# Kernel optimization log

Hardware: AMD Instinct MI355X
Metric: run time of the kernel (lower is better)

## Reference

```python
import jax, jax.numpy as jnp
import numpy as np
import math

DIM_MODEL = 1024
N_HEAD = 16
NUM_NEURON = 64
MAX_LEN = 2048
B, S = 4, 2048


def setup_inputs() -> dict:
    key = jax.random.key(0)
    ks = jax.random.split(key, 11)
    d, p = DIM_MODEL, N_HEAD * NUM_NEURON
    sc_in = 1.0 / math.sqrt(d)
    sc_p = 1.0 / math.sqrt(p)
    return {
        "q": jax.random.normal(ks[0], (B, S, d), jnp.float32),
        "k": jax.random.normal(ks[1], (B, S, d), jnp.float32),
        "v": jax.random.normal(ks[2], (B, S, d), jnp.float32),
        "Wq": jax.random.normal(ks[3], (d, p), jnp.float32) * sc_in,
        "bq": jnp.zeros((p,), jnp.float32),
        "Wk": jax.random.normal(ks[4], (d, p), jnp.float32) * sc_in,
        "bk": jnp.zeros((p,), jnp.float32),
        "Wv": jax.random.normal(ks[5], (d, p), jnp.float32) * sc_in,
        "bv": jnp.zeros((p,), jnp.float32),
        "Wf": jax.random.normal(ks[6], (p, d), jnp.float32) * sc_p,
        "bf": jnp.zeros((d,), jnp.float32),
    }


def _split_heads(x):  # [B,S,H*Dh] -> [B,H,S,Dh]
    b, s, _ = x.shape
    return x.reshape(b, s, N_HEAD, NUM_NEURON).transpose(0, 2, 1, 3)


def reference(q, k, v, Wq, bq, Wk, bk, Wv, bv, Wf, bf):
    qh = _split_heads(q @ Wq + bq)
    kh = _split_heads(k @ Wk + bk)
    vh = _split_heads(v @ Wv + bv)
    # NOTE: original scales by 1/sqrt(max_len), not 1/sqrt(head_dim)
    scores = jnp.einsum("bhqd,bhkd->bhqk", qh, kh) / math.sqrt(MAX_LEN)
    s = scores.shape[-1]
    causal = jnp.tril(jnp.ones((s, s), bool))  # [S,S]
    scores = jnp.where(causal[None, None], scores, -jnp.inf)
    attn = jax.nn.softmax(scores, axis=-1)
    out = jnp.einsum("bhqk,bhkd->bhqd", attn, vh)  # [B,H,S,Dh]
    c = out.transpose(0, 2, 1, 3).reshape(out.shape[0], out.shape[2], N_HEAD * NUM_NEURON)
    return c @ Wf + bf
```

## Files before the change

kernel.cpp:

```cpp
#include <hip/hip_runtime.h>
#include <stdint.h>

#define DMODEL 1024
#define NHEAD 16
#define DH 64
#define BB 4
#define SS 2048
#define MROWS (BB * SS)

typedef __bf16 bfx8 __attribute__((ext_vector_type(8)));
typedef float f32x4 __attribute__((ext_vector_type(4)));
typedef float fvec4 __attribute__((ext_vector_type(4)));
typedef int i32x4 __attribute__((ext_vector_type(4)));
typedef unsigned short u16x8 __attribute__((ext_vector_type(8)));
typedef unsigned short u16x4 __attribute__((ext_vector_type(4)));

__device__ __forceinline__ unsigned short f2bf(float f) {
    union { float f; unsigned int u; } v; v.f = f;
    unsigned int r = v.u + 0x7FFFu + ((v.u >> 16) & 1u);
    return (unsigned short)(r >> 16);
}

__device__ __forceinline__ unsigned int cvtpk(float lo, float hi) {
    unsigned int r;
    asm("v_cvt_pk_bf16_f32 %0, %1, %2" : "=v"(r) : "v"(lo), "v"(hi));
    return r;
}

typedef __attribute__((address_space(1))) const void gas_t;
typedef __attribute__((address_space(3))) void las_t;
__device__ __forceinline__ void gload_lds16(const void* g, void* l) {
    __builtin_amdgcn_global_load_lds((gas_t*)g, (las_t*)l, 16, 0, 0);
}

__device__ __forceinline__ int sigma_k(int i) {
    return (i & 0x20) | ((i & 0x0C) << 1) | ((i & 0x10) >> 2) | (i & 3);
}

__global__ void cvt3_kernel(const float* __restrict__ s0, const float* __restrict__ s1,
                            const float* __restrict__ s2,
                            unsigned short* __restrict__ d0, unsigned short* __restrict__ d1,
                            unsigned short* __restrict__ d2, int n8)
{
    const float* s = (blockIdx.y == 0) ? s0 : (blockIdx.y == 1) ? s1 : s2;
    unsigned short* d = (blockIdx.y == 0) ? d0 : (blockIdx.y == 1) ? d1 : d2;
    int i = blockIdx.x * blockDim.x + threadIdx.x;
    if (i >= n8) return;
    fvec4 a = *reinterpret_cast<const fvec4*>(&s[(size_t)i * 8]);
    fvec4 b = *reinterpret_cast<const fvec4*>(&s[(size_t)i * 8 + 4]);
    u16x8 o;
    #pragma unroll
    for (int j = 0; j < 4; ++j) { o[j] = f2bf(a[j]); o[j + 4] = f2bf(b[j]); }
    *reinterpret_cast<u16x8*>(&d[(size_t)i * 8]) = o;
}

__global__ void transpose_cvt3_kernel(const float* __restrict__ W0, unsigned short* __restrict__ T0,
                                      const float* __restrict__ W1, unsigned short* __restrict__ T1,
                                      const float* __restrict__ W2, unsigned short* __restrict__ T2)
{
    const float* W = (blockIdx.z == 0) ? W0 : (blockIdx.z == 1) ? W1 : W2;
    unsigned short* Wt = (blockIdx.z == 0) ? T0 : (blockIdx.z == 1) ? T1 : T2;
    __shared__ unsigned short t[64][72];
    const int tid = threadIdx.x;
    const int r0 = blockIdx.y * 64, c0 = blockIdx.x * 64;
    #pragma unroll
    for (int i = 0; i < 4; ++i) {
        int idx = tid + i * 256;
        int r = idx >> 4, c4 = idx & 15;
        fvec4 v = *reinterpret_cast<const fvec4*>(&W[(size_t)(r0 + r) * DMODEL + c0 + c4 * 4]);
        #pragma unroll
        for (int j = 0; j < 4; ++j) t[c4 * 4 + j][r] = f2bf(v[j]);
    }
    __syncthreads();
    #pragma unroll
    for (int i = 0; i < 2; ++i) {
        int idx = tid + i * 256;
        int r = idx >> 3, c8 = idx & 7;
        u16x8 v = *reinterpret_cast<const u16x8*>(&t[r][c8 * 8]);
        *reinterpret_cast<u16x8*>(&Wt[(size_t)(c0 + r) * DMODEL + r0 + c8 * 8]) = v;
    }
}

struct GArg {
    const unsigned short* A;
    const unsigned short* Bt;
    const float* bias;
    void* O;
    float osc;
    int mode;
};

__global__ __launch_bounds__(256, 4)
void gemm_kernel(GArg g0, GArg g1, int M, int N, int K)
{
    const GArg g = blockIdx.z ? g1 : g0;
    __shared__ unsigned short sA[128 * 64];
    __shared__ unsigned short sB[128 * 64];
    const int tid  = threadIdx.x;
    const int lane = tid & 63;
    const int wave = tid >> 6;
    const int wm = (wave >> 1) * 64, wn = (wave & 1) * 64;
    const int m0 = blockIdx.x * 128, n0 = blockIdx.y * 128;
    const int lr = lane & 15;
    const int lg = lane >> 4;

    f32x4 acc[4][4] = {};

    for (int kk0 = 0; kk0 < K; kk0 += 64) {
        __syncthreads();
        #pragma unroll
        for (int i = 0; i < 4; ++i) {
            int c = tid + i * 256;
            int row = c >> 3, col8 = c & 7;
            gload_lds16(&g.A[(size_t)(m0 + row) * K + kk0 + col8 * 8], &sA[c * 8]);
        }
        #pragma unroll
        for (int i = 0; i < 4; ++i) {
            int c = tid + i * 256;
            int row = c >> 3, col8 = c & 7;
            gload_lds16(&g.Bt[(size_t)(n0 + row) * K + kk0 + col8 * 8], &sB[c * 8]);
        }
        __syncthreads();

        #pragma unroll
        for (int kk = 0; kk < 2; ++kk) {
            bfx8 af[4], bfr[4];
            #pragma unroll
            for (int m = 0; m < 4; ++m)
                af[m] = *reinterpret_cast<const bfx8*>(
                    &sA[(wm + m * 16 + lr) * 64 + kk * 32 + lg * 8]);
            #pragma unroll
            for (int n = 0; n < 4; ++n)
                bfr[n] = *reinterpret_cast<const bfx8*>(
                    &sB[(wn + n * 16 + lr) * 64 + kk * 32 + lg * 8]);
            #pragma unroll
            for (int m = 0; m < 4; ++m)
                #pragma unroll
                for (int n = 0; n < 4; ++n)
                    acc[m][n] = __builtin_amdgcn_mfma_f32_16x16x32_bf16(
                        af[m], bfr[n], acc[m][n], 0, 0, 0);
        }
    }

    #pragma unroll
    for (int n = 0; n < 4; ++n) {
        int col = n0 + wn + n * 16 + lr;
        float bv = g.bias[col];
        #pragma unroll
        for (int m = 0; m < 4; ++m) {
            int rowb = m0 + wm + m * 16 + lg * 4;
            float val[4];
            #pragma unroll
            for (int r = 0; r < 4; ++r) val[r] = (acc[m][n][r] + bv) * g.osc;
            if (g.mode == 0) {
                #pragma unroll
                for (int r = 0; r < 4; ++r)
                    ((unsigned short*)g.O)[(size_t)(rowb + r) * N + col] = f2bf(val[r]);
            } else if (g.mode == 2) {
                #pragma unroll
                for (int r = 0; r < 4; ++r)
                    ((float*)g.O)[(size_t)(rowb + r) * N + col] = val[r];
            } else {
                int bq = rowb >> 11, s = rowb & 2047;
                int hh = col >> 6, d = col & 63;
                u16x4 pk;
                #pragma unroll
                for (int r = 0; r < 4; ++r) pk[r] = f2bf(val[r]);
                size_t idx = ((size_t)(bq * 16 + hh) * 64 + d) * 2048 + s;
                *reinterpret_cast<u16x4*>(&((unsigned short*)g.O)[idx]) = pk;
            }
        }
    }
}

__global__ __launch_bounds__(512, 4)
void attn_kernel(const unsigned short* __restrict__ Q,
                 const unsigned short* __restrict__ K,
                 const unsigned short* __restrict__ Vt,
                 unsigned short* __restrict__ C)
{
    __shared__ unsigned short sK[2][8192];
    __shared__ unsigned short sV[2][8192];

    const int tid  = threadIdx.x;
    const int lane = tid & 63;
    const int wave = tid >> 6;
    const int lr = lane & 15, lg = lane >> 4;
    const int bh = blockIdx.x;
    const int p  = blockIdx.y;
    const int b = bh >> 4, h = bh & 15;
    const size_t rowbase = (size_t)b * SS;
    const int hcol = h * DH;

    const int srow = tid >> 3, sc8 = tid & 7;
    const int sig  = sigma_k(srow);
    const int woff = srow * 64 + ((sc8 ^ (srow & 7)) * 8);
    const int p0 = lg ^ (lr & 7);

    const u16x8 onesu = {0x3F80, 0x3F80, 0x3F80, 0x3F80, 0x3F80, 0x3F80, 0x3F80, 0x3F80};
    union { u16x8 u; bfx8 b; } onesc; onesc.u = onesu;
    const bfx8 ones = onesc.b;

    #pragma unroll
    for (int ph = 0; ph < 2; ++ph) {
        const int qt = ph ? p : (15 - p);
        const int q0 = qt * 128;

        bfx8 aq[2];
        {
            int qr = q0 + wave * 16 + lr;
            const unsigned short* qp = &Q[(rowbase + qr) * DMODEL + hcol + lg * 8];
            aq[0] = *reinterpret_cast<const bfx8*>(qp);
            aq[1] = *reinterpret_cast<const bfx8*>(qp + 32);
        }

        float m_run = 0.f;
        f32x4 acc_l = {};
        f32x4 acc_o[4] = {};
        bool mz = true;
        const int qmax_wave = q0 + wave * 16 + 15;
        const int npairs = qt + 1;

        u16x8 rk[2], rv[2];
        #pragma unroll
        for (int s = 0; s < 2; ++s) {
            rk[s] = *reinterpret_cast<const u16x8*>(
                &K[(rowbase + s * 64 + sig) * DMODEL + hcol + sc8 * 8]);
            rv[s] = *reinterpret_cast<const u16x8*>(
                &Vt[((size_t)bh * DH + srow) * SS + s * 64 + sc8 * 8]);
        }
        #pragma unroll
        for (int s = 0; s < 2; ++s) {
            *reinterpret_cast<u16x8*>(&sK[0][s * 4096 + woff]) = rk[s];
            *reinterpret_cast<u16x8*>(&sV[0][s * 4096 + woff]) = rv[s];
        }
        if (npairs > 1) {
            #pragma unroll
            for (int s = 0; s < 2; ++s) {
                const int kk = (2 + s) * 64;
                rk[s] = *reinterpret_cast<const u16x8*>(
                    &K[(rowbase + kk + sig) * DMODEL + hcol + sc8 * 8]);
                rv[s] = *reinterpret_cast<const u16x8*>(
                    &Vt[((size_t)bh * DH + srow) * SS + kk + sc8 * 8]);
            }
        }
        __syncthreads();

        for (int u = 0; u < npairs; ++u) {
            const int cur = u & 1;
            #pragma unroll
            for (int s = 0; s < 2; ++s) {
                const int k0 = (2 * u + s) * 64;
                if (k0 > qmax_wave) break;

                f32x4 sc[4];
                __builtin_amdgcn_s_setprio(1);
                #pragma unroll
                for (int nf = 0; nf < 4; ++nf) {
                    int i = nf * 16 + lr;
                    bfx8 ak0 = *reinterpret_cast<const bfx8*>(&sK[cur][s * 4096 + i * 64 + p0 * 8]);
                    bfx8 ak1 = *reinterpret_cast<const bfx8*>(&sK[cur][s * 4096 + i * 64 + (p0 ^ 4) * 8]);
                    f32x4 sv = {0.f, 0.f, 0.f, 0.f};
                    sv = __builtin_amdgcn_mfma_f32_16x16x32_bf16(ak0, aq[0], sv, 0, 0, 0);
                    sv = __builtin_amdgcn_mfma_f32_16x16x32_bf16(ak1, aq[1], sv, 0, 0, 0);
                    sc[nf] = sv;
                }
                __builtin_amdgcn_s_setprio(0);
                if (k0 + 63 > q0 + wave * 16) {
                    int qrow = q0 + wave * 16 + lr;
                    #pragma unroll
                    for (int nf = 0; nf < 4; ++nf) {
                        int kb = k0 + ((nf >> 1) << 5) + (lg << 3) + ((nf & 1) << 2);
                        #pragma unroll
                        for (int r = 0; r < 4; ++r)
                            if (kb + r > qrow) sc[nf][r] = -3.0e38f;
                    }
                }
                float a0 = fmaxf(fmaxf(sc[0][0], sc[0][1]), sc[0][2]);
                float a1 = fmaxf(fmaxf(sc[0][3], sc[1][0]), sc[1][1]);
                float a2 = fmaxf(fmaxf(sc[1][2], sc[1][3]), sc[2][0]);
                float a3 = fmaxf(fmaxf(sc[2][1], sc[2][2]), sc[2][3]);
                float a4 = fmaxf(fmaxf(sc[3][0], sc[3][1]), sc[3][2]);
                float pmax = fmaxf(fmaxf(fmaxf(a0, a1), fmaxf(a2, a3)),
                                   fmaxf(a4, sc[3][3]));
                if (mz && __all(pmax <= 8.0f)) {
                    #pragma unroll
                    for (int nf = 0; nf < 4; ++nf)
                        #pragma unroll
                        for (int r = 0; r < 4; ++r)
                            sc[nf][r] = __builtin_exp2f(sc[nf][r]);
                } else {
                    mz = false;
                    float mx = pmax;
                    mx = fmaxf(mx, __shfl_xor(mx, 16, 64));
                    mx = fmaxf(mx, __shfl_xor(mx, 32, 64));
                    float mnew = fmaxf(m_run, mx);
                    float fs = __builtin_exp2f(m_run - mnew);
                    m_run = mnew;
                    #pragma unroll
                    for (int nf = 0; nf < 4; ++nf)
                        #pragma unroll
                        for (int r = 0; r < 4; ++r)
                            sc[nf][r] = __builtin_exp2f(sc[nf][r] - mnew);
                    #pragma unroll
                    for (int r = 0; r < 4; ++r) {
                        float fsa = __shfl(fs, lg * 4 + r, 64);
                        #pragma unroll
                        for (int d = 0; d < 4; ++d) acc_o[d][r] *= fsa;
                        acc_l[r] *= fsa;
                    }
                }
                #pragma unroll
                for (int h2 = 0; h2 < 2; ++h2) {
                    union { i32x4 i; bfx8 b; } pa;
                    pa.i[0] = cvtpk(sc[2 * h2][0],     sc[2 * h2][1]);
                    pa.i[1] = cvtpk(sc[2 * h2][2],     sc[2 * h2][3]);
                    pa.i[2] = cvtpk(sc[2 * h2 + 1][0], sc[2 * h2 + 1][1]);
                    pa.i[3] = cvtpk(sc[2 * h2 + 1][2], sc[2 * h2 + 1][3]);
                    __builtin_amdgcn_s_setprio(1);
                    acc_l = __builtin_amdgcn_mfma_f32_16x16x32_bf16(pa.b, ones, acc_l, 0, 0, 0);
                    #pragma unroll
                    for (int d = 0; d < 4; ++d) {
                        int i = d * 16 + lr;
                        int pv = ((h2 << 2) | lg) ^ (lr & 7);
                        bfx8 bv0 = *reinterpret_cast<const bfx8*>(&sV[cur][s * 4096 + i * 64 + pv * 8]);
                        acc_o[d] = __builtin_amdgcn_mfma_f32_16x16x32_bf16(pa.b, bv0, acc_o[d], 0, 0, 0);
                    }
                    __builtin_amdgcn_s_setprio(0);
                }
            }
            if (u + 1 < npairs) {
                #pragma unroll
                for (int s = 0; s < 2; ++s) {
                    *reinterpret_cast<u16x8*>(&sK[cur ^ 1][s * 4096 + woff]) = rk[s];
                    *reinterpret_cast<u16x8*>(&sV[cur ^ 1][s * 4096 + woff]) = rv[s];
                }
                if (u + 2 < npairs) {
                    #pragma unroll
                    for (int s = 0; s < 2; ++s) {
                        const int kk = (2 * u + 4 + s) * 64;
                        rk[s] = *reinterpret_cast<const u16x8*>(
                            &K[(rowbase + kk + sig) * DMODEL + hcol + sc8 * 8]);
                        rv[s] = *reinterpret_cast<const u16x8*>(
                            &Vt[((size_t)bh * DH + srow) * SS + kk + sc8 * 8]);
                    }
                }
            }
            __syncthreads();
        }

        f32x4 linv;
        #pragma unroll
        for (int r = 0; r < 4; ++r) linv[r] = 1.0f / acc_l[r];
        const int qrb = q0 + wave * 16 + lg * 4;
        #pragma unroll
        for (int d = 0; d < 4; ++d) {
            int col = hcol + d * 16 + lr;
            #pragma unroll
            for (int r = 0; r < 4; ++r)
                C[(rowbase + qrb + r) * DMODEL + col] = f2bf(acc_o[d][r] * linv[r]);
        }
    }
}

extern "C" void kernel_launch(void* const* d_in, const int* in_sizes, int n_in,
                              void* d_out, int out_size, void* d_ws, size_t ws_size,
                              hipStream_t stream)
{
    const float* q  = (const float*)d_in[0];
    const float* k  = (const float*)d_in[1];
    const float* v  = (const float*)d_in[2];
    const float* Wq = (const float*)d_in[3];
    const float* bq = (const float*)d_in[4];
    const float* Wk = (const float*)d_in[5];
    const float* bk = (const float*)d_in[6];
    const float* Wv = (const float*)d_in[7];
    const float* bv = (const float*)d_in[8];
    const float* Wf = (const float*)d_in[9];
    const float* bf = (const float*)d_in[10];

    unsigned short* ws = (unsigned short*)d_ws;
    const size_t SZ = (size_t)MROWS * DMODEL;
    unsigned short* ws0 = ws;
    unsigned short* ws1 = ws + SZ;
    unsigned short* ws2 = ws + 2 * SZ;
    unsigned short* ws3 = ws + 3 * SZ;

    unsigned short* scr = (unsigned short*)d_out;
    unsigned short* WqT = scr;
    unsigned short* WkT = scr + 1048576;
    unsigned short* WvT = scr + 2097152;
    unsigned short* Qb  = scr + 4194304;

    const float qscale = 0.02209708691207961f * 1.44269504088896341f;

    const int n8 = (int)(SZ / 8);
    cvt3_kernel<<<dim3((n8 + 255) / 256, 3), 256, 0, stream>>>(q, k, v, ws0, ws1, ws2, n8);

    transpose_cvt3_kernel<<<dim3(16, 16, 3), 256, 0, stream>>>(Wq, WqT, Wk, WkT, Wv, WvT);

    {
        GArg gq{ws0, WqT, bq, Qb,  qscale, 0};
        GArg gk{ws1, WkT, bk, ws3, 1.0f,   0};
        gemm_kernel<<<dim3(64, 8, 2), 256, 0, stream>>>(gq, gk, MROWS, DMODEL, DMODEL);
    }
    {
        GArg gv{ws2, WvT, bv, ws0, 1.0f, 3};
        gemm_kernel<<<dim3(64, 8, 1), 256, 0, stream>>>(gv, gv, MROWS, DMODEL, DMODEL);
    }
    transpose_cvt3_kernel<<<dim3(16, 16, 1), 256, 0, stream>>>(Wf, ws2, Wf, ws2, Wf, ws2);

    attn_kernel<<<dim3(BB * NHEAD, 8), 512, 0, stream>>>(Qb, ws3, ws0, ws1);

    {
        GArg gf{ws1, ws2, bf, (float*)d_out, 1.0f, 2};
        gemm_kernel<<<dim3(64, 8, 1), 256, 0, stream>>>(gf, gf, MROWS, DMODEL, DMODEL);
    }
}
```

Measured before the change: 193.3 us.

## Fuse fp32-to-bf16 input conversion into projection GEMM and merge launches

Drops the separate conversion pass over q, k and v. The projection GEMM now reads the fp32 activations directly and packs them to bf16 before storing to shared memory. The Q, K and V projections run in one three-slice launch, and all four weight transposes run in one launch, so fewer kernels are launched and the bf16 copies are never written or re-read. The catch is that the A tile now goes through registers with plain global loads instead of direct global-to-LDS loads, and each A element is read again by every N-tile block as fp32, which moves twice the bytes.

```diff
diff --git a/kernel.cpp b/kernel.cpp
--- a/kernel.cpp
+++ b/kernel.cpp
@@ -37,29 +37,15 @@
     return (i & 0x20) | ((i & 0x0C) << 1) | ((i & 0x10) >> 2) | (i & 3);
 }
 
-__global__ void cvt3_kernel(const float* __restrict__ s0, const float* __restrict__ s1,
-                            const float* __restrict__ s2,
-                            unsigned short* __restrict__ d0, unsigned short* __restrict__ d1,
-                            unsigned short* __restrict__ d2, int n8)
+__global__ void transpose_cvt4_kernel(const float* __restrict__ W0, unsigned short* __restrict__ T0,
+                                      const float* __restrict__ W1, unsigned short* __restrict__ T1,
+                                      const float* __restrict__ W2, unsigned short* __restrict__ T2,
+                                      const float* __restrict__ W3, unsigned short* __restrict__ T3)
 {
-    const float* s = (blockIdx.y == 0) ? s0 : (blockIdx.y == 1) ? s1 : s2;
-    unsigned short* d = (blockIdx.y == 0) ? d0 : (blockIdx.y == 1) ? d1 : d2;
-    int i = blockIdx.x * blockDim.x + threadIdx.x;
-    if (i >= n8) return;
-    fvec4 a = *reinterpret_cast<const fvec4*>(&s[(size_t)i * 8]);
-    fvec4 b = *reinterpret_cast<const fvec4*>(&s[(size_t)i * 8 + 4]);
-    u16x8 o;
-    #pragma unroll
-    for (int j = 0; j < 4; ++j) { o[j] = f2bf(a[j]); o[j + 4] = f2bf(b[j]); }
-    *reinterpret_cast<u16x8*>(&d[(size_t)i * 8]) = o;
-}
-
-__global__ void transpose_cvt3_kernel(const float* __restrict__ W0, unsigned short* __restrict__ T0,
-                                      const float* __restrict__ W1, unsigned short* __restrict__ T1,
-                                      const float* __restrict__ W2, unsigned short* __restrict__ T2)
-{
-    const float* W = (blockIdx.z == 0) ? W0 : (blockIdx.z == 1) ? W1 : W2;
-    unsigned short* Wt = (blockIdx.z == 0) ? T0 : (blockIdx.z == 1) ? T1 : T2;
+    const float* W = (blockIdx.z == 0) ? W0 : (blockIdx.z == 1) ? W1
+                   : (blockIdx.z == 2) ? W2 : W3;
+    unsigned short* Wt = (blockIdx.z == 0) ? T0 : (blockIdx.z == 1) ? T1
+                       : (blockIdx.z == 2) ? T2 : T3;
     __shared__ unsigned short t[64][72];
     const int tid = threadIdx.x;
     const int r0 = blockIdx.y * 64, c0 = blockIdx.x * 64;
@@ -82,7 +68,7 @@
 }
 
 struct GArg {
-    const unsigned short* A;
+    const void* A;
     const unsigned short* Bt;
     const float* bias;
     void* O;
@@ -90,10 +76,11 @@
     int mode;
 };
 
+template<bool A_FP32>
 __global__ __launch_bounds__(256, 4)
-void gemm_kernel(GArg g0, GArg g1, int M, int N, int K)
+void gemm_kernel(GArg g0, GArg g1, GArg g2, int M, int N, int K)
 {
-    const GArg g = blockIdx.z ? g1 : g0;
+    const GArg g = (blockIdx.z == 0) ? g0 : (blockIdx.z == 1) ? g1 : g2;
     __shared__ unsigned short sA[128 * 64];
     __shared__ unsigned short sB[128 * 64];
     const int tid  = threadIdx.x;
@@ -108,11 +95,30 @@
 
     for (int kk0 = 0; kk0 < K; kk0 += 64) {
         __syncthreads();
-        #pragma unroll
-        for (int i = 0; i < 4; ++i) {
-            int c = tid + i * 256;
-            int row = c >> 3, col8 = c & 7;
-            gload_lds16(&g.A[(size_t)(m0 + row) * K + kk0 + col8 * 8], &sA[c * 8]);
+        if (A_FP32) {
+            const float* Af = (const float*)g.A;
+            #pragma unroll
+            for (int i = 0; i < 4; ++i) {
+                int c = tid + i * 256;
+                int row = c >> 3, col8 = c & 7;
+                const float* src = &Af[(size_t)(m0 + row) * K + kk0 + col8 * 8];
+                fvec4 x = *reinterpret_cast<const fvec4*>(src);
+                fvec4 y = *reinterpret_cast<const fvec4*>(src + 4);
+                union { i32x4 i; u16x8 u; } pk;
+                pk.i[0] = cvtpk(x[0], x[1]);
+                pk.i[1] = cvtpk(x[2], x[3]);
+                pk.i[2] = cvtpk(y[0], y[1]);
+                pk.i[3] = cvtpk(y[2], y[3]);
+                *reinterpret_cast<u16x8*>(&sA[c * 8]) = pk.u;
+            }
+        } else {
+            const unsigned short* Ab = (const unsigned short*)g.A;
+            #pragma unroll
+            for (int i = 0; i < 4; ++i) {
+                int c = tid + i * 256;
+                int row = c >> 3, col8 = c & 7;
+                gload_lds16(&Ab[(size_t)(m0 + row) * K + kk0 + col8 * 8], &sA[c * 8]);
+            }
         }
         #pragma unroll
         for (int i = 0; i < 4; ++i) {
@@ -381,39 +387,35 @@
 
     unsigned short* ws = (unsigned short*)d_ws;
     const size_t SZ = (size_t)MROWS * DMODEL;
-    unsigned short* ws0 = ws;
-    unsigned short* ws1 = ws + SZ;
-    unsigned short* ws2 = ws + 2 * SZ;
-    unsigned short* ws3 = ws + 3 * SZ;
+    unsigned short* Vt = ws;
+    unsigned short* Cb = ws + SZ;
+    unsigned short* Kb = ws + 3 * SZ;
 
     unsigned short* scr = (unsigned short*)d_out;
     unsigned short* WqT = scr;
     unsigned short* WkT = scr + 1048576;
     unsigned short* WvT = scr + 2097152;
+    unsigned short* WfT = scr + 3145728;
     unsigned short* Qb  = scr + 4194304;
 
     const float qscale = 0.02209708691207961f * 1.44269504088896341f;
 
-    const int n8 = (int)(SZ / 8);
-    cvt3_kernel<<<dim3((n8 + 255) / 256, 3), 256, 0, stream>>>(q, k, v, ws0, ws1, ws2, n8);
-
-    transpose_cvt3_kernel<<<dim3(16, 16, 3), 256, 0, stream>>>(Wq, WqT, Wk, WkT, Wv, WvT);
+    transpose_cvt4_kernel<<<dim3(16, 16, 4), 256, 0, stream>>>(
+        Wq, WqT, Wk, WkT, Wv, WvT, Wf, WfT);
 
     {
-        GArg gq{ws0, WqT, bq, Qb,  qscale, 0};
-        GArg gk{ws1, WkT, bk, ws3, 1.0f,   0};
-        gemm_kernel<<<dim3(64, 8, 2), 256, 0, stream>>>(gq, gk, MROWS, DMODEL, DMODEL);
-    }
+        GArg gq{q, WqT, bq, Qb, qscale, 0};
+        GArg gk{k, WkT, bk, Kb, 1.0f,   0};
+        GArg gv{v, WvT, bv, Vt, 1.0f,   3};
+        gemm_kernel<true><<<dim3(64, 8, 3), 256, 0, stream>>>(
+            gq, gk, gv, MROWS, DMODEL, DMODEL);
+    }
+
+    attn_kernel<<<dim3(BB * NHEAD, 8), 512, 0, stream>>>(Qb, Kb, Vt, Cb);
+
     {
-        GArg gv{ws2, WvT, bv, ws0, 1.0f, 3};
-        gemm_kernel<<<dim3(64, 8, 1), 256, 0, stream>>>(gv, gv, MROWS, DMODEL, DMODEL);
-    }
-    transpose_cvt3_kernel<<<dim3(16, 16, 1), 256, 0, stream>>>(Wf, ws2, Wf, ws2, Wf, ws2);
-
-    attn_kernel<<<dim3(BB * NHEAD, 8), 512, 0, stream>>>(Qb, ws3, ws0, ws1);
-
-    {
-        GArg gf{ws1, ws2, bf, (float*)d_out, 1.0f, 2};
-        gemm_kernel<<<dim3(64, 8, 1), 256, 0, stream>>>(gf, gf, MROWS, DMODEL, DMODEL);
-    }
-}
+        GArg gf{Cb, WfT, bf, (float*)d_out, 1.0f, 2};
+        gemm_kernel<false><<<dim3(64, 8, 1), 256, 0, stream>>>(
+            gf, gf, gf, MROWS, DMODEL, DMODEL);
+    }
+}
```

New measurement: 185.2 us. -4.2%, faster.
